# Optimization experiments

Measured on AMD Instinct MI355X. Metric: run time of the kernel, lower is better.

## Reference

```python
import jax, jax.numpy as jnp
import numpy as np

G = 8          # grid_size
DH = 32        # dim_head
EPS = 1e-5
INIT_LS = 1e-5


def setup_inputs() -> dict:
    key = jax.random.key(0)
    ks = jax.random.split(key, 8)
    B, H, W, C = 16, 128, 128, 256
    s = 1.0 / np.sqrt(C)
    return {
        "x": jax.random.normal(ks[0], (B, H, W, C), dtype=jnp.float32),
        "ln_w": jnp.ones((C,), jnp.float32),
        "ln_b": jnp.zeros((C,), jnp.float32),
        "in_proj_w": jax.random.uniform(ks[1], (3 * C, C), jnp.float32, -s, s),
        "in_proj_b": jnp.zeros((3 * C,), jnp.float32),
        "out_proj_w": jax.random.uniform(ks[2], (C, C), jnp.float32, -s, s),
        "out_proj_b": jnp.zeros((C,), jnp.float32),
        "gamma": jnp.full((C,), INIT_LS, jnp.float32),
    }


def _grid_attention(x, ln_w, ln_b, in_proj_w, in_proj_b, out_proj_w, out_proj_b, gamma):
    B, H, W, C = x.shape
    nh = C // DH
    # LayerNorm over channels
    mu = jnp.mean(x, axis=-1, keepdims=True)
    var = jnp.mean(jnp.square(x - mu), axis=-1, keepdims=True)
    x = (x - mu) * jax.lax.rsqrt(var + EPS) * ln_w + ln_b
    # grid partition: (B,G,H/G,G,W/G,C) -> (B,H/G,W/G,G,G,C) -> (N, G*G, C)
    hg, wg = H // G, W // G
    xw = x.reshape(B, G, hg, G, wg, C).transpose(0, 2, 4, 1, 3, 5)
    xw = xw.reshape(B * hg * wg, G * G, C)  # N windows of L=G*G tokens
    # MHSA (nn.MultiheadAttention semantics)
    qkv = xw @ in_proj_w.T + in_proj_b                      # (N, L, 3C)
    q, k, v = jnp.split(qkv, 3, axis=-1)
    N, L = xw.shape[0], xw.shape[1]
    q = q.reshape(N, L, nh, DH).transpose(0, 2, 1, 3)        # (N, nh, L, DH)
    k = k.reshape(N, L, nh, DH).transpose(0, 2, 1, 3)
    v = v.reshape(N, L, nh, DH).transpose(0, 2, 1, 3)
    scores = jnp.einsum("nhld,nhmd->nhlm", q, k) / np.sqrt(DH)
    attn = jax.nn.softmax(scores, axis=-1)
    out = jnp.einsum("nhlm,nhmd->nhld", attn, v)             # (N, nh, L, DH)
    out = out.transpose(0, 2, 1, 3).reshape(N, L, C)
    out = out @ out_proj_w.T + out_proj_b
    # LayerScale
    out = out * gamma
    # grid reverse: (B,H/G,W/G,G,G,C) -> (B,G,H/G,G,W/G,C) -> (B,H,W,C)
    out = out.reshape(B, hg, wg, G, G, C).transpose(0, 3, 1, 4, 2, 5)
    return out.reshape(B, H, W, C)


def reference(x, ln_w, ln_b, in_proj_w, in_proj_b, out_proj_w, out_proj_b, gamma):
    return _grid_attention(x, ln_w, ln_b, in_proj_w, in_proj_b,
                           out_proj_w, out_proj_b, gamma)
```

## Files before the change

### kernel.cpp

```cpp
#include <hip/hip_runtime.h>

typedef __attribute__((ext_vector_type(8))) short short8;
typedef __attribute__((ext_vector_type(4))) float f32x4;
typedef __attribute__((ext_vector_type(4))) unsigned short us4;

__device__ __forceinline__ unsigned short f2b(float f) {
  unsigned int u = __float_as_uint(f);
  u += 0x7FFFu + ((u >> 16) & 1u);
  return (unsigned short)(u >> 16);
}

__global__ void prep_weights(const float* __restrict__ wq,
                             const float* __restrict__ wo,
                             unsigned short* __restrict__ dst) {
  int idx = blockIdx.x * blockDim.x + threadIdx.x;
  int e = idx * 4;
  float4 v;
  if (e < 196608) v = *(const float4*)(wq + e);
  else            v = *(const float4*)(wo + (e - 196608));
  us4 o;
  o.x = f2b(v.x); o.y = f2b(v.y); o.z = f2b(v.z); o.w = f2b(v.w);
  *(us4*)(dst + e) = o;
}

__global__ __launch_bounds__(512, 4) void grid_attn(
    const float* __restrict__ x,
    const float* __restrict__ ln_w,
    const float* __restrict__ ln_b,
    const unsigned short* __restrict__ Wqkv,
    const float* __restrict__ bqkv,
    const unsigned short* __restrict__ Wout,
    const float* __restrict__ bout,
    const float* __restrict__ gamma,
    float* __restrict__ out) {

  __shared__ unsigned short ldsX[64 * 264];
  __shared__ unsigned short ldsB[8][1152];

  const int tid = threadIdx.x;
  const int w   = tid >> 6;
  const int lid = tid & 63;
  const int l16 = lid & 15;
  const int lhi = lid >> 4;

  const int n  = blockIdx.x;
  const int b  = n >> 8;
  const int wi = (n >> 4) & 15;
  const int wj = n & 15;

  {
    float4 lwv = *(const float4*)(ln_w + lid * 4);
    float4 lbv = *(const float4*)(ln_b + lid * 4);
    #pragma unroll
    for (int t = 0; t < 8; ++t) {
      int l  = w * 8 + t;
      int a  = l >> 3, cg = l & 7;
      int hh = a * 16 + wi, ww = cg * 16 + wj;
      const float4 v = *(const float4*)(x + ((size_t)((b * 128 + hh) * 128 + ww)) * 256 + lid * 4);
      float s1 = v.x + v.y + v.z + v.w;
      float s2 = v.x * v.x + v.y * v.y + v.z * v.z + v.w * v.w;
      #pragma unroll
      for (int m = 32; m >= 1; m >>= 1) {
        s1 += __shfl_xor(s1, m);
        s2 += __shfl_xor(s2, m);
      }
      float mu  = s1 * (1.0f / 256.0f);
      float var = s2 * (1.0f / 256.0f) - mu * mu;
      float rs  = rsqrtf(var + 1e-5f);
      us4 o;
      o.x = f2b((v.x - mu) * rs * lwv.x + lbv.x);
      o.y = f2b((v.y - mu) * rs * lwv.y + lbv.y);
      o.z = f2b((v.z - mu) * rs * lwv.z + lbv.z);
      o.w = f2b((v.w - mu) * rs * lwv.w + lbv.w);
      *(us4*)(&ldsX[l * 264 + lid * 4]) = o;
    }
  }
  __syncthreads();

  unsigned short* bb = &ldsB[w][0];

  f32x4 qa[2][4], ka[2][4];
  #pragma unroll
  for (int dt = 0; dt < 2; ++dt)
    #pragma unroll
    for (int tt = 0; tt < 4; ++tt) {
      qa[dt][tt] = (f32x4){0.f, 0.f, 0.f, 0.f};
      ka[dt][tt] = (f32x4){0.f, 0.f, 0.f, 0.f};
    }
  #pragma unroll
  for (int kc = 0; kc < 8; ++kc) {
    short8 xf[4];
    #pragma unroll
    for (int tt = 0; tt < 4; ++tt)
      xf[tt] = *(const short8*)(&ldsX[(tt * 16 + l16) * 264 + kc * 32 + lhi * 8]);
    short8 wq[2], wk[2];
    #pragma unroll
    for (int dt = 0; dt < 2; ++dt) {
      wq[dt] = *(const short8*)(&Wqkv[(size_t)(w * 32 + dt * 16 + l16) * 256 + kc * 32 + lhi * 8]);
      wk[dt] = *(const short8*)(&Wqkv[(size_t)(256 + w * 32 + dt * 16 + l16) * 256 + kc * 32 + lhi * 8]);
    }
    #pragma unroll
    for (int dt = 0; dt < 2; ++dt)
      #pragma unroll
      for (int tt = 0; tt < 4; ++tt) {
        qa[dt][tt] = __builtin_amdgcn_mfma_f32_16x16x32_bf16(wq[dt], xf[tt], qa[dt][tt], 0, 0, 0);
        ka[dt][tt] = __builtin_amdgcn_mfma_f32_16x16x32_bf16(wk[dt], xf[tt], ka[dt][tt], 0, 0, 0);
      }
  }

  short8 qf[4], kf[4];
  {
    f32x4 bqv[2], bkv[2];
    #pragma unroll
    for (int dt = 0; dt < 2; ++dt) {
      bqv[dt] = *(const f32x4*)(bqkv + w * 32 + dt * 16 + lhi * 4);
      bkv[dt] = *(const f32x4*)(bqkv + 256 + w * 32 + dt * 16 + lhi * 4);
    }
    #pragma unroll
    for (int tt = 0; tt < 4; ++tt) {
      #pragma unroll
      for (int dt = 0; dt < 2; ++dt)
        #pragma unroll
        for (int r = 0; r < 4; ++r)
          bb[l16 * 40 + dt * 16 + lhi * 4 + r] = f2b(qa[dt][tt][r] + bqv[dt][r]);
      qf[tt] = *(const short8*)(&bb[l16 * 40 + lhi * 8]);
    }
    #pragma unroll
    for (int tt = 0; tt < 4; ++tt) {
      #pragma unroll
      for (int dt = 0; dt < 2; ++dt)
        #pragma unroll
        for (int r = 0; r < 4; ++r)
          bb[l16 * 40 + dt * 16 + lhi * 4 + r] = f2b(ka[dt][tt][r] + bkv[dt][r]);
      kf[tt] = *(const short8*)(&bb[l16 * 40 + lhi * 8]);
    }
  }

  f32x4 sc[4][4];
  #pragma unroll
  for (int m = 0; m < 4; ++m)
    #pragma unroll
    for (int nn = 0; nn < 4; ++nn)
      sc[m][nn] = __builtin_amdgcn_mfma_f32_16x16x32_bf16(kf[m], qf[nn], (f32x4){0.f,0.f,0.f,0.f}, 0, 0, 0);

  short8 pf[4][2];
  const float scale = 0.17677669529663687f;
  #pragma unroll
  for (int nn = 0; nn < 4; ++nn) {
    float mx = sc[0][nn][0];
    #pragma unroll
    for (int m = 0; m < 4; ++m)
      #pragma unroll
      for (int r = 0; r < 4; ++r)
        mx = fmaxf(mx, sc[m][nn][r]);
    mx = fmaxf(mx, __shfl_xor(mx, 16));
    mx = fmaxf(mx, __shfl_xor(mx, 32));
    float e[4][4], sum = 0.f;
    #pragma unroll
    for (int m = 0; m < 4; ++m)
      #pragma unroll
      for (int r = 0; r < 4; ++r) {
        e[m][r] = __expf((sc[m][nn][r] - mx) * scale);
        sum += e[m][r];
      }
    sum += __shfl_xor(sum, 16);
    sum += __shfl_xor(sum, 32);
    float inv = 1.0f / sum;
    #pragma unroll
    for (int m = 0; m < 4; ++m)
      #pragma unroll
      for (int r = 0; r < 4; ++r)
        bb[l16 * 72 + m * 16 + lhi * 4 + r] = f2b(e[m][r] * inv);
    pf[nn][0] = *(const short8*)(&bb[l16 * 72 + lhi * 8]);
    pf[nn][1] = *(const short8*)(&bb[l16 * 72 + 32 + lhi * 8]);
  }

  f32x4 va[4][2];
  #pragma unroll
  for (int tt = 0; tt < 4; ++tt)
    #pragma unroll
    for (int dt = 0; dt < 2; ++dt)
      va[tt][dt] = (f32x4){0.f, 0.f, 0.f, 0.f};
  #pragma unroll
  for (int kc = 0; kc < 8; ++kc) {
    short8 xf[4];
    #pragma unroll
    for (int tt = 0; tt < 4; ++tt)
      xf[tt] = *(const short8*)(&ldsX[(tt * 16 + l16) * 264 + kc * 32 + lhi * 8]);
    short8 wv[2];
    #pragma unroll
    for (int dt = 0; dt < 2; ++dt)
      wv[dt] = *(const short8*)(&Wqkv[(size_t)(512 + w * 32 + dt * 16 + l16) * 256 + kc * 32 + lhi * 8]);
    #pragma unroll
    for (int tt = 0; tt < 4; ++tt)
      #pragma unroll
      for (int dt = 0; dt < 2; ++dt)
        va[tt][dt] = __builtin_amdgcn_mfma_f32_16x16x32_bf16(xf[tt], wv[dt], va[tt][dt], 0, 0, 0);
  }

  short8 vf[2][2];
  {
    float bvs[2];
    #pragma unroll
    for (int dt = 0; dt < 2; ++dt) bvs[dt] = bqkv[512 + w * 32 + dt * 16 + l16];
    #pragma unroll
    for (int dt = 0; dt < 2; ++dt) {
      #pragma unroll
      for (int tt = 0; tt < 4; ++tt)
        #pragma unroll
        for (int r = 0; r < 4; ++r)
          bb[l16 * 72 + tt * 16 + lhi * 4 + r] = f2b(va[tt][dt][r] + bvs[dt]);
      vf[dt][0] = *(const short8*)(&bb[l16 * 72 + lhi * 8]);
      vf[dt][1] = *(const short8*)(&bb[l16 * 72 + 32 + lhi * 8]);
    }
  }

  f32x4 oa[4][2];
  #pragma unroll
  for (int nn = 0; nn < 4; ++nn)
    #pragma unroll
    for (int dt = 0; dt < 2; ++dt)
      oa[nn][dt] = (f32x4){0.f, 0.f, 0.f, 0.f};
  #pragma unroll
  for (int kc = 0; kc < 2; ++kc)
    #pragma unroll
    for (int nn = 0; nn < 4; ++nn)
      #pragma unroll
      for (int dt = 0; dt < 2; ++dt)
        oa[nn][dt] = __builtin_amdgcn_mfma_f32_16x16x32_bf16(pf[nn][kc], vf[dt][kc], oa[nn][dt], 0, 0, 0);

  __syncthreads();

  #pragma unroll
  for (int nn = 0; nn < 4; ++nn)
    #pragma unroll
    for (int dt = 0; dt < 2; ++dt)
      #pragma unroll
      for (int r = 0; r < 4; ++r)
        ldsX[(nn * 16 + lhi * 4 + r) * 264 + w * 32 + dt * 16 + l16] = f2b(oa[nn][dt][r]);
  __syncthreads();

  f32x4 ya[4][2];
  #pragma unroll
  for (int mt = 0; mt < 4; ++mt)
    #pragma unroll
    for (int nt = 0; nt < 2; ++nt)
      ya[mt][nt] = (f32x4){0.f, 0.f, 0.f, 0.f};
  #pragma unroll
  for (int kc = 0; kc < 8; ++kc) {
    short8 af[4];
    #pragma unroll
    for (int mt = 0; mt < 4; ++mt)
      af[mt] = *(const short8*)(&ldsX[(mt * 16 + l16) * 264 + kc * 32 + lhi * 8]);
    short8 wf[2];
    #pragma unroll
    for (int nt = 0; nt < 2; ++nt)
      wf[nt] = *(const short8*)(&Wout[(size_t)(w * 32 + nt * 16 + l16) * 256 + kc * 32 + lhi * 8]);
    #pragma unroll
    for (int mt = 0; mt < 4; ++mt)
      #pragma unroll
      for (int nt = 0; nt < 2; ++nt)
        ya[mt][nt] = __builtin_amdgcn_mfma_f32_16x16x32_bf16(af[mt], wf[nt], ya[mt][nt], 0, 0, 0);
  }

  float ob0 = bout[w * 32 + l16];
  float ob1 = bout[w * 32 + 16 + l16];
  float g0  = gamma[w * 32 + l16];
  float g1  = gamma[w * 32 + 16 + l16];
  #pragma unroll
  for (int mt = 0; mt < 4; ++mt)
    #pragma unroll
    for (int r = 0; r < 4; ++r) {
      int row = mt * 16 + lhi * 4 + r;
      int a = row >> 3, cg = row & 7;
      int hh = a * 16 + wi, ww2 = cg * 16 + wj;
      float* po = out + ((size_t)((b * 128 + hh) * 128 + ww2)) * 256 + w * 32;
      po[l16]      = (ya[mt][0][r] + ob0) * g0;
      po[l16 + 16] = (ya[mt][1][r] + ob1) * g1;
    }
}

extern "C" void kernel_launch(void* const* d_in, const int* in_sizes, int n_in,
                              void* d_out, int out_size, void* d_ws, size_t ws_size,
                              hipStream_t stream) {
  const float* x    = (const float*)d_in[0];
  const float* ln_w = (const float*)d_in[1];
  const float* ln_b = (const float*)d_in[2];
  const float* ipw  = (const float*)d_in[3];
  const float* ipb  = (const float*)d_in[4];
  const float* opw  = (const float*)d_in[5];
  const float* opb  = (const float*)d_in[6];
  const float* gm   = (const float*)d_in[7];

  unsigned short* wbf = (unsigned short*)d_ws;

  prep_weights<<<256, 256, 0, stream>>>(ipw, opw, wbf);
  grid_attn<<<4096, 512, 0, stream>>>(x, ln_w, ln_b,
                                      wbf, ipb,
                                      wbf + 196608, opb,
                                      gm, (float*)d_out);
}
```

Measured before the change: 358.8 us.

## Fold LayerNorm and LayerScale into weights; replace LDS transposes with permlane swaps

LayerNorm's affine terms and gamma are now folded into the bf16 weights and precomputed bias vectors in a prep kernel. The main kernel stores raw bf16 x and applies mean/rstd as a rank-1 correction after the QKV GEMM. The per-row reductions are batched with a shuffle transpose, and the accumulator-to-operand layout changes for Q/K/P/V go through v_permlane swaps instead of per-wave LDS scratch. The attention output is computed transposed so it can be written with packed stores. Rounding x to bf16 before normalisation changes numerics and can lose accuracy when the mean is large.

```diff
diff --git a/kernel.cpp b/kernel.cpp
--- a/kernel.cpp
+++ b/kernel.cpp
@@ -1,41 +1,77 @@
 #include <hip/hip_runtime.h>
+#include <hip/hip_bf16.h>
 
 typedef __attribute__((ext_vector_type(8))) short short8;
 typedef __attribute__((ext_vector_type(4))) float f32x4;
 typedef __attribute__((ext_vector_type(4))) unsigned short us4;
+typedef __attribute__((ext_vector_type(2))) unsigned uint2v;
+
+union U8 { unsigned u[4]; short8 s; };
 
 __device__ __forceinline__ unsigned short f2b(float f) {
-  unsigned int u = __float_as_uint(f);
+  unsigned u = __float_as_uint(f);
   u += 0x7FFFu + ((u >> 16) & 1u);
   return (unsigned short)(u >> 16);
 }
-
-__global__ void prep_weights(const float* __restrict__ wq,
-                             const float* __restrict__ wo,
-                             unsigned short* __restrict__ dst) {
-  int idx = blockIdx.x * blockDim.x + threadIdx.x;
-  int e = idx * 4;
-  float4 v;
-  if (e < 196608) v = *(const float4*)(wq + e);
-  else            v = *(const float4*)(wo + (e - 196608));
-  us4 o;
-  o.x = f2b(v.x); o.y = f2b(v.y); o.z = f2b(v.z); o.w = f2b(v.w);
-  *(us4*)(dst + e) = o;
+__device__ __forceinline__ float b2f(unsigned short h) {
+  return __uint_as_float((unsigned)h << 16);
+}
+__device__ __forceinline__ unsigned pkbf(float lo, float hi) {
+  __hip_bfloat162 h = __float22bfloat162_rn(make_float2(lo, hi));
+  unsigned u; __builtin_memcpy(&u, &h, 4);
+  return u;
+}
+__device__ __forceinline__ void swp32(unsigned &a, unsigned &b) {
+  asm("v_permlane32_swap_b32 %0, %1" : "+v"(a), "+v"(b));
+}
+__device__ __forceinline__ void swp16(unsigned &a, unsigned &b) {
+  asm("v_permlane16_swap_b32 %0, %1" : "+v"(a), "+v"(b));
+}
+
+__global__ __launch_bounds__(64) void prep(
+    const float* __restrict__ wq, const float* __restrict__ wo,
+    const float* __restrict__ lnw, const float* __restrict__ lnb,
+    const float* __restrict__ bqkv, const float* __restrict__ bo,
+    const float* __restrict__ gm,
+    unsigned short* __restrict__ wbf, float* __restrict__ Sarr,
+    float* __restrict__ Carr, float* __restrict__ boG) {
+  int d = blockIdx.x, lane = threadIdx.x;
+  if (d < 768) {
+    float4 wv = *(const float4*)(wq + (size_t)d * 256 + lane * 4);
+    float4 lw = *(const float4*)(lnw + lane * 4);
+    float4 lb = *(const float4*)(lnb + lane * 4);
+    us4 o;
+    o.x = f2b(wv.x * lw.x); o.y = f2b(wv.y * lw.y);
+    o.z = f2b(wv.z * lw.z); o.w = f2b(wv.w * lw.w);
+    *(us4*)(wbf + (size_t)d * 256 + lane * 4) = o;
+    float s = b2f(o.x) + b2f(o.y) + b2f(o.z) + b2f(o.w);
+    float c = wv.x * lb.x + wv.y * lb.y + wv.z * lb.z + wv.w * lb.w;
+    #pragma unroll
+    for (int m = 32; m >= 1; m >>= 1) { s += __shfl_xor(s, m); c += __shfl_xor(c, m); }
+    if (lane == 0) { Sarr[d] = s; Carr[d] = c + bqkv[d]; }
+  } else {
+    int dd = d - 768;
+    float g = gm[dd];
+    float4 wv = *(const float4*)(wo + (size_t)dd * 256 + lane * 4);
+    us4 o;
+    o.x = f2b(wv.x * g); o.y = f2b(wv.y * g); o.z = f2b(wv.z * g); o.w = f2b(wv.w * g);
+    *(us4*)(wbf + 196608 + (size_t)dd * 256 + lane * 4) = o;
+    if (lane == 0) boG[dd] = bo[dd] * g;
+  }
 }
 
 __global__ __launch_bounds__(512, 4) void grid_attn(
     const float* __restrict__ x,
-    const float* __restrict__ ln_w,
-    const float* __restrict__ ln_b,
     const unsigned short* __restrict__ Wqkv,
-    const float* __restrict__ bqkv,
     const unsigned short* __restrict__ Wout,
-    const float* __restrict__ bout,
-    const float* __restrict__ gamma,
+    const float* __restrict__ Sarr,
+    const float* __restrict__ Carr,
+    const float* __restrict__ boG,
     float* __restrict__ out) {
 
   __shared__ unsigned short ldsX[64 * 264];
-  __shared__ unsigned short ldsB[8][1152];
+  __shared__ float ldsMu[64];
+  __shared__ float ldsRs[64];
 
   const int tid = threadIdx.x;
   const int w   = tid >> 6;
@@ -49,35 +85,54 @@
   const int wj = n & 15;
 
   {
-    float4 lwv = *(const float4*)(ln_w + lid * 4);
-    float4 lbv = *(const float4*)(ln_b + lid * 4);
+    float2 p[8];
     #pragma unroll
     for (int t = 0; t < 8; ++t) {
-      int l  = w * 8 + t;
-      int a  = l >> 3, cg = l & 7;
+      int l = w * 8 + t;
+      int a = l >> 3, cg = l & 7;
       int hh = a * 16 + wi, ww = cg * 16 + wj;
-      const float4 v = *(const float4*)(x + ((size_t)((b * 128 + hh) * 128 + ww)) * 256 + lid * 4);
-      float s1 = v.x + v.y + v.z + v.w;
-      float s2 = v.x * v.x + v.y * v.y + v.z * v.z + v.w * v.w;
-      #pragma unroll
-      for (int m = 32; m >= 1; m >>= 1) {
-        s1 += __shfl_xor(s1, m);
-        s2 += __shfl_xor(s2, m);
-      }
-      float mu  = s1 * (1.0f / 256.0f);
-      float var = s2 * (1.0f / 256.0f) - mu * mu;
-      float rs  = rsqrtf(var + 1e-5f);
-      us4 o;
-      o.x = f2b((v.x - mu) * rs * lwv.x + lbv.x);
-      o.y = f2b((v.y - mu) * rs * lwv.y + lbv.y);
-      o.z = f2b((v.z - mu) * rs * lwv.z + lbv.z);
-      o.w = f2b((v.w - mu) * rs * lwv.w + lbv.w);
-      *(us4*)(&ldsX[l * 264 + lid * 4]) = o;
+      float4 v = *(const float4*)(x + ((size_t)((b * 128 + hh) * 128 + ww)) * 256 + lid * 4);
+      p[t].x = v.x + v.y + v.z + v.w;
+      p[t].y = v.x * v.x + v.y * v.y + v.z * v.z + v.w * v.w;
+      uint2v o; o.x = pkbf(v.x, v.y); o.y = pkbf(v.z, v.w);
+      *(uint2v*)(&ldsX[l * 264 + lid * 4]) = o;
+    }
+    const int h1 = lid & 1, h2 = (lid >> 1) & 1, h4 = (lid >> 2) & 1;
+    float2 q[4];
+    #pragma unroll
+    for (int i = 0; i < 4; ++i) {
+      float sx = h1 ? p[i].x : p[i + 4].x, sy = h1 ? p[i].y : p[i + 4].y;
+      float kx = h1 ? p[i + 4].x : p[i].x, ky = h1 ? p[i + 4].y : p[i].y;
+      q[i].x = kx + __shfl_xor(sx, 1);
+      q[i].y = ky + __shfl_xor(sy, 1);
+    }
+    float2 r2[2];
+    #pragma unroll
+    for (int i = 0; i < 2; ++i) {
+      float sx = h2 ? q[i].x : q[i + 2].x, sy = h2 ? q[i].y : q[i + 2].y;
+      float kx = h2 ? q[i + 2].x : q[i].x, ky = h2 ? q[i + 2].y : q[i].y;
+      r2[i].x = kx + __shfl_xor(sx, 2);
+      r2[i].y = ky + __shfl_xor(sy, 2);
+    }
+    float fx, fy;
+    {
+      float sx = h4 ? r2[0].x : r2[1].x, sy = h4 ? r2[0].y : r2[1].y;
+      float kx = h4 ? r2[1].x : r2[0].x, ky = h4 ? r2[1].y : r2[0].y;
+      fx = kx + __shfl_xor(sx, 4);
+      fy = ky + __shfl_xor(sy, 4);
+    }
+    fx += __shfl_xor(fx, 8);  fy += __shfl_xor(fy, 8);
+    fx += __shfl_xor(fx, 16); fy += __shfl_xor(fy, 16);
+    fx += __shfl_xor(fx, 32); fy += __shfl_xor(fy, 32);
+    if (lid < 8) {
+      int T = h1 * 4 + h2 * 2 + h4;
+      float mu = fx * (1.0f / 256.0f);
+      float var = fy * (1.0f / 256.0f) - mu * mu;
+      ldsMu[w * 8 + T] = mu;
+      ldsRs[w * 8 + T] = rsqrtf(var + 1e-5f);
     }
   }
   __syncthreads();
-
-  unsigned short* bb = &ldsB[w][0];
 
   f32x4 qa[2][4], ka[2][4];
   #pragma unroll
@@ -87,52 +142,66 @@
       qa[dt][tt] = (f32x4){0.f, 0.f, 0.f, 0.f};
       ka[dt][tt] = (f32x4){0.f, 0.f, 0.f, 0.f};
     }
-  #pragma unroll
-  for (int kc = 0; kc < 8; ++kc) {
-    short8 xf[4];
-    #pragma unroll
-    for (int tt = 0; tt < 4; ++tt)
-      xf[tt] = *(const short8*)(&ldsX[(tt * 16 + l16) * 264 + kc * 32 + lhi * 8]);
-    short8 wq[2], wk[2];
-    #pragma unroll
-    for (int dt = 0; dt < 2; ++dt) {
-      wq[dt] = *(const short8*)(&Wqkv[(size_t)(w * 32 + dt * 16 + l16) * 256 + kc * 32 + lhi * 8]);
-      wk[dt] = *(const short8*)(&Wqkv[(size_t)(256 + w * 32 + dt * 16 + l16) * 256 + kc * 32 + lhi * 8]);
-    }
-    #pragma unroll
-    for (int dt = 0; dt < 2; ++dt)
+  {
+    const unsigned short* wqp = Wqkv + (size_t)(w * 32 + l16) * 256 + lhi * 8;
+    const unsigned short* wkp = wqp + 256 * 256;
+    #pragma unroll
+    for (int kc = 0; kc < 8; ++kc) {
+      short8 xf[4];
+      #pragma unroll
+      for (int tt = 0; tt < 4; ++tt)
+        xf[tt] = *(const short8*)(&ldsX[(tt * 16 + l16) * 264 + kc * 32 + lhi * 8]);
+      short8 wq0 = *(const short8*)(wqp + kc * 32);
+      short8 wq1 = *(const short8*)(wqp + 16 * 256 + kc * 32);
+      short8 wk0 = *(const short8*)(wkp + kc * 32);
+      short8 wk1 = *(const short8*)(wkp + 16 * 256 + kc * 32);
       #pragma unroll
       for (int tt = 0; tt < 4; ++tt) {
-        qa[dt][tt] = __builtin_amdgcn_mfma_f32_16x16x32_bf16(wq[dt], xf[tt], qa[dt][tt], 0, 0, 0);
-        ka[dt][tt] = __builtin_amdgcn_mfma_f32_16x16x32_bf16(wk[dt], xf[tt], ka[dt][tt], 0, 0, 0);
-      }
+        qa[0][tt] = __builtin_amdgcn_mfma_f32_16x16x32_bf16(wq0, xf[tt], qa[0][tt], 0, 0, 0);
+        qa[1][tt] = __builtin_amdgcn_mfma_f32_16x16x32_bf16(wq1, xf[tt], qa[1][tt], 0, 0, 0);
+        ka[0][tt] = __builtin_amdgcn_mfma_f32_16x16x32_bf16(wk0, xf[tt], ka[0][tt], 0, 0, 0);
+        ka[1][tt] = __builtin_amdgcn_mfma_f32_16x16x32_bf16(wk1, xf[tt], ka[1][tt], 0, 0, 0);
+      }
+    }
   }
 
   short8 qf[4], kf[4];
   {
-    f32x4 bqv[2], bkv[2];
-    #pragma unroll
-    for (int dt = 0; dt < 2; ++dt) {
-      bqv[dt] = *(const f32x4*)(bqkv + w * 32 + dt * 16 + lhi * 4);
-      bkv[dt] = *(const f32x4*)(bqkv + 256 + w * 32 + dt * 16 + lhi * 4);
-    }
+    f32x4 Sq0 = *(const f32x4*)(Sarr + w * 32 + lhi * 4);
+    f32x4 Sq1 = *(const f32x4*)(Sarr + w * 32 + 16 + lhi * 4);
+    f32x4 Cq0 = *(const f32x4*)(Carr + w * 32 + lhi * 4);
+    f32x4 Cq1 = *(const f32x4*)(Carr + w * 32 + 16 + lhi * 4);
+    f32x4 Sk0 = *(const f32x4*)(Sarr + 256 + w * 32 + lhi * 4);
+    f32x4 Sk1 = *(const f32x4*)(Sarr + 256 + w * 32 + 16 + lhi * 4);
+    f32x4 Ck0 = *(const f32x4*)(Carr + 256 + w * 32 + lhi * 4);
+    f32x4 Ck1 = *(const f32x4*)(Carr + 256 + w * 32 + 16 + lhi * 4);
     #pragma unroll
     for (int tt = 0; tt < 4; ++tt) {
-      #pragma unroll
-      for (int dt = 0; dt < 2; ++dt)
-        #pragma unroll
-        for (int r = 0; r < 4; ++r)
-          bb[l16 * 40 + dt * 16 + lhi * 4 + r] = f2b(qa[dt][tt][r] + bqv[dt][r]);
-      qf[tt] = *(const short8*)(&bb[l16 * 40 + lhi * 8]);
-    }
-    #pragma unroll
-    for (int tt = 0; tt < 4; ++tt) {
-      #pragma unroll
-      for (int dt = 0; dt < 2; ++dt)
-        #pragma unroll
-        for (int r = 0; r < 4; ++r)
-          bb[l16 * 40 + dt * 16 + lhi * 4 + r] = f2b(ka[dt][tt][r] + bkv[dt][r]);
-      kf[tt] = *(const short8*)(&bb[l16 * 40 + lhi * 8]);
+      float rs  = ldsRs[tt * 16 + l16];
+      float nmu = -ldsMu[tt * 16 + l16];
+      float e0[4], e1[4];
+      #pragma unroll
+      for (int r = 0; r < 4; ++r) {
+        e0[r] = fmaf(rs, fmaf(nmu, Sq0[r], qa[0][tt][r]), Cq0[r]);
+        e1[r] = fmaf(rs, fmaf(nmu, Sq1[r], qa[1][tt][r]), Cq1[r]);
+      }
+      unsigned a0 = pkbf(e0[0], e0[1]), a1 = pkbf(e0[2], e0[3]);
+      unsigned a2 = pkbf(e1[0], e1[1]), a3 = pkbf(e1[2], e1[3]);
+      swp32(a0, a2); swp32(a1, a3);
+      swp16(a0, a2); swp16(a1, a3);
+      U8 z; z.u[0] = a0; z.u[1] = a1; z.u[2] = a2; z.u[3] = a3;
+      qf[tt] = z.s;
+      #pragma unroll
+      for (int r = 0; r < 4; ++r) {
+        e0[r] = fmaf(rs, fmaf(nmu, Sk0[r], ka[0][tt][r]), Ck0[r]);
+        e1[r] = fmaf(rs, fmaf(nmu, Sk1[r], ka[1][tt][r]), Ck1[r]);
+      }
+      unsigned c0 = pkbf(e0[0], e0[1]), c1 = pkbf(e0[2], e0[3]);
+      unsigned c2 = pkbf(e1[0], e1[1]), c3 = pkbf(e1[2], e1[3]);
+      swp32(c0, c2); swp32(c1, c3);
+      swp16(c0, c2); swp16(c1, c3);
+      U8 y; y.u[0] = c0; y.u[1] = c1; y.u[2] = c2; y.u[3] = c3;
+      kf[tt] = y.s;
     }
   }
 
@@ -141,9 +210,9 @@
   for (int m = 0; m < 4; ++m)
     #pragma unroll
     for (int nn = 0; nn < 4; ++nn)
-      sc[m][nn] = __builtin_amdgcn_mfma_f32_16x16x32_bf16(kf[m], qf[nn], (f32x4){0.f,0.f,0.f,0.f}, 0, 0, 0);
-
-  short8 pf[4][2];
+      sc[m][nn] = __builtin_amdgcn_mfma_f32_16x16x32_bf16(kf[m], qf[nn], (f32x4){0.f, 0.f, 0.f, 0.f}, 0, 0, 0);
+
+  short8 ptf[4][2];
   const float scale = 0.17677669529663687f;
   #pragma unroll
   for (int nn = 0; nn < 4; ++nn) {
@@ -166,13 +235,19 @@
     sum += __shfl_xor(sum, 16);
     sum += __shfl_xor(sum, 32);
     float inv = 1.0f / sum;
-    #pragma unroll
-    for (int m = 0; m < 4; ++m)
-      #pragma unroll
-      for (int r = 0; r < 4; ++r)
-        bb[l16 * 72 + m * 16 + lhi * 4 + r] = f2b(e[m][r] * inv);
-    pf[nn][0] = *(const short8*)(&bb[l16 * 72 + lhi * 8]);
-    pf[nn][1] = *(const short8*)(&bb[l16 * 72 + 32 + lhi * 8]);
+    unsigned bu[8];
+    #pragma unroll
+    for (int m = 0; m < 4; ++m) {
+      bu[m * 2]     = pkbf(e[m][0] * inv, e[m][1] * inv);
+      bu[m * 2 + 1] = pkbf(e[m][2] * inv, e[m][3] * inv);
+    }
+    swp32(bu[0], bu[2]); swp32(bu[1], bu[3]); swp32(bu[4], bu[6]); swp32(bu[5], bu[7]);
+    swp16(bu[0], bu[2]); swp16(bu[1], bu[3]); swp16(bu[4], bu[6]); swp16(bu[5], bu[7]);
+    U8 z0, z1;
+    z0.u[0] = bu[0]; z0.u[1] = bu[1]; z0.u[2] = bu[2]; z0.u[3] = bu[3];
+    z1.u[0] = bu[4]; z1.u[1] = bu[5]; z1.u[2] = bu[6]; z1.u[3] = bu[7];
+    ptf[nn][0] = z0.s;
+    ptf[nn][1] = z1.s;
   }
 
   f32x4 va[4][2];
@@ -181,63 +256,84 @@
     #pragma unroll
     for (int dt = 0; dt < 2; ++dt)
       va[tt][dt] = (f32x4){0.f, 0.f, 0.f, 0.f};
-  #pragma unroll
-  for (int kc = 0; kc < 8; ++kc) {
-    short8 xf[4];
-    #pragma unroll
-    for (int tt = 0; tt < 4; ++tt)
-      xf[tt] = *(const short8*)(&ldsX[(tt * 16 + l16) * 264 + kc * 32 + lhi * 8]);
-    short8 wv[2];
-    #pragma unroll
-    for (int dt = 0; dt < 2; ++dt)
-      wv[dt] = *(const short8*)(&Wqkv[(size_t)(512 + w * 32 + dt * 16 + l16) * 256 + kc * 32 + lhi * 8]);
-    #pragma unroll
-    for (int tt = 0; tt < 4; ++tt)
-      #pragma unroll
-      for (int dt = 0; dt < 2; ++dt)
-        va[tt][dt] = __builtin_amdgcn_mfma_f32_16x16x32_bf16(xf[tt], wv[dt], va[tt][dt], 0, 0, 0);
-  }
-
-  short8 vf[2][2];
-  {
-    float bvs[2];
-    #pragma unroll
-    for (int dt = 0; dt < 2; ++dt) bvs[dt] = bqkv[512 + w * 32 + dt * 16 + l16];
+  {
+    const unsigned short* wvp = Wqkv + (size_t)(512 + w * 32 + l16) * 256 + lhi * 8;
+    #pragma unroll
+    for (int kc = 0; kc < 8; ++kc) {
+      short8 xf[4];
+      #pragma unroll
+      for (int tt = 0; tt < 4; ++tt)
+        xf[tt] = *(const short8*)(&ldsX[(tt * 16 + l16) * 264 + kc * 32 + lhi * 8]);
+      short8 wv0 = *(const short8*)(wvp + kc * 32);
+      short8 wv1 = *(const short8*)(wvp + 16 * 256 + kc * 32);
+      #pragma unroll
+      for (int tt = 0; tt < 4; ++tt) {
+        va[tt][0] = __builtin_amdgcn_mfma_f32_16x16x32_bf16(xf[tt], wv0, va[tt][0], 0, 0, 0);
+        va[tt][1] = __builtin_amdgcn_mfma_f32_16x16x32_bf16(xf[tt], wv1, va[tt][1], 0, 0, 0);
+      }
+    }
+  }
+
+  short8 vtf[2][2];
+  {
+    f32x4 rs4[4], nmu4[4];
+    #pragma unroll
+    for (int tt = 0; tt < 4; ++tt) {
+      rs4[tt] = *(const f32x4*)(&ldsRs[tt * 16 + lhi * 4]);
+      f32x4 m4 = *(const f32x4*)(&ldsMu[tt * 16 + lhi * 4]);
+      nmu4[tt] = -m4;
+    }
     #pragma unroll
     for (int dt = 0; dt < 2; ++dt) {
+      float Sv = Sarr[512 + w * 32 + dt * 16 + l16];
+      float Cv = Carr[512 + w * 32 + dt * 16 + l16];
+      float vv[4][4];
       #pragma unroll
       for (int tt = 0; tt < 4; ++tt)
         #pragma unroll
         for (int r = 0; r < 4; ++r)
-          bb[l16 * 72 + tt * 16 + lhi * 4 + r] = f2b(va[tt][dt][r] + bvs[dt]);
-      vf[dt][0] = *(const short8*)(&bb[l16 * 72 + lhi * 8]);
-      vf[dt][1] = *(const short8*)(&bb[l16 * 72 + 32 + lhi * 8]);
-    }
-  }
-
-  f32x4 oa[4][2];
+          vv[tt][r] = fmaf(rs4[tt][r], fmaf(nmu4[tt][r], Sv, va[tt][dt][r]), Cv);
+      unsigned bu[8];
+      #pragma unroll
+      for (int tt = 0; tt < 4; ++tt) {
+        bu[tt * 2]     = pkbf(vv[tt][0], vv[tt][1]);
+        bu[tt * 2 + 1] = pkbf(vv[tt][2], vv[tt][3]);
+      }
+      swp32(bu[0], bu[2]); swp32(bu[1], bu[3]); swp32(bu[4], bu[6]); swp32(bu[5], bu[7]);
+      swp16(bu[0], bu[2]); swp16(bu[1], bu[3]); swp16(bu[4], bu[6]); swp16(bu[5], bu[7]);
+      U8 z0, z1;
+      z0.u[0] = bu[0]; z0.u[1] = bu[1]; z0.u[2] = bu[2]; z0.u[3] = bu[3];
+      z1.u[0] = bu[4]; z1.u[1] = bu[5]; z1.u[2] = bu[6]; z1.u[3] = bu[7];
+      vtf[dt][0] = z0.s;
+      vtf[dt][1] = z1.s;
+    }
+  }
+
+  f32x4 ot[2][4];
+  #pragma unroll
+  for (int dt = 0; dt < 2; ++dt)
+    #pragma unroll
+    for (int nn = 0; nn < 4; ++nn)
+      ot[dt][nn] = (f32x4){0.f, 0.f, 0.f, 0.f};
+  #pragma unroll
+  for (int kc = 0; kc < 2; ++kc)
+    #pragma unroll
+    for (int dt = 0; dt < 2; ++dt)
+      #pragma unroll
+      for (int nn = 0; nn < 4; ++nn)
+        ot[dt][nn] = __builtin_amdgcn_mfma_f32_16x16x32_bf16(vtf[dt][kc], ptf[nn][kc], ot[dt][nn], 0, 0, 0);
+
+  __syncthreads();
+
   #pragma unroll
   for (int nn = 0; nn < 4; ++nn)
     #pragma unroll
-    for (int dt = 0; dt < 2; ++dt)
-      oa[nn][dt] = (f32x4){0.f, 0.f, 0.f, 0.f};
-  #pragma unroll
-  for (int kc = 0; kc < 2; ++kc)
-    #pragma unroll
-    for (int nn = 0; nn < 4; ++nn)
-      #pragma unroll
-      for (int dt = 0; dt < 2; ++dt)
-        oa[nn][dt] = __builtin_amdgcn_mfma_f32_16x16x32_bf16(pf[nn][kc], vf[dt][kc], oa[nn][dt], 0, 0, 0);
-
-  __syncthreads();
-
-  #pragma unroll
-  for (int nn = 0; nn < 4; ++nn)
-    #pragma unroll
-    for (int dt = 0; dt < 2; ++dt)
-      #pragma unroll
-      for (int r = 0; r < 4; ++r)
-        ldsX[(nn * 16 + lhi * 4 + r) * 264 + w * 32 + dt * 16 + l16] = f2b(oa[nn][dt][r]);
+    for (int dt = 0; dt < 2; ++dt) {
+      uint2v o;
+      o.x = pkbf(ot[dt][nn][0], ot[dt][nn][1]);
+      o.y = pkbf(ot[dt][nn][2], ot[dt][nn][3]);
+      *(uint2v*)(&ldsX[(nn * 16 + l16) * 264 + w * 32 + dt * 16 + lhi * 4]) = o;
+    }
   __syncthreads();
 
   f32x4 ya[4][2];
@@ -246,27 +342,26 @@
     #pragma unroll
     for (int nt = 0; nt < 2; ++nt)
       ya[mt][nt] = (f32x4){0.f, 0.f, 0.f, 0.f};
-  #pragma unroll
-  for (int kc = 0; kc < 8; ++kc) {
-    short8 af[4];
-    #pragma unroll
-    for (int mt = 0; mt < 4; ++mt)
-      af[mt] = *(const short8*)(&ldsX[(mt * 16 + l16) * 264 + kc * 32 + lhi * 8]);
-    short8 wf[2];
-    #pragma unroll
-    for (int nt = 0; nt < 2; ++nt)
-      wf[nt] = *(const short8*)(&Wout[(size_t)(w * 32 + nt * 16 + l16) * 256 + kc * 32 + lhi * 8]);
-    #pragma unroll
-    for (int mt = 0; mt < 4; ++mt)
-      #pragma unroll
-      for (int nt = 0; nt < 2; ++nt)
-        ya[mt][nt] = __builtin_amdgcn_mfma_f32_16x16x32_bf16(af[mt], wf[nt], ya[mt][nt], 0, 0, 0);
-  }
-
-  float ob0 = bout[w * 32 + l16];
-  float ob1 = bout[w * 32 + 16 + l16];
-  float g0  = gamma[w * 32 + l16];
-  float g1  = gamma[w * 32 + 16 + l16];
+  {
+    const unsigned short* wop = Wout + (size_t)(w * 32 + l16) * 256 + lhi * 8;
+    #pragma unroll
+    for (int kc = 0; kc < 8; ++kc) {
+      short8 af[4];
+      #pragma unroll
+      for (int mt = 0; mt < 4; ++mt)
+        af[mt] = *(const short8*)(&ldsX[(mt * 16 + l16) * 264 + kc * 32 + lhi * 8]);
+      short8 wf0 = *(const short8*)(wop + kc * 32);
+      short8 wf1 = *(const short8*)(wop + 16 * 256 + kc * 32);
+      #pragma unroll
+      for (int mt = 0; mt < 4; ++mt) {
+        ya[mt][0] = __builtin_amdgcn_mfma_f32_16x16x32_bf16(af[mt], wf0, ya[mt][0], 0, 0, 0);
+        ya[mt][1] = __builtin_amdgcn_mfma_f32_16x16x32_bf16(af[mt], wf1, ya[mt][1], 0, 0, 0);
+      }
+    }
+  }
+
+  float ob0 = boG[w * 32 + l16];
+  float ob1 = boG[w * 32 + 16 + l16];
   #pragma unroll
   for (int mt = 0; mt < 4; ++mt)
     #pragma unroll
@@ -275,8 +370,8 @@
       int a = row >> 3, cg = row & 7;
       int hh = a * 16 + wi, ww2 = cg * 16 + wj;
       float* po = out + ((size_t)((b * 128 + hh) * 128 + ww2)) * 256 + w * 32;
-      po[l16]      = (ya[mt][0][r] + ob0) * g0;
-      po[l16 + 16] = (ya[mt][1][r] + ob1) * g1;
+      po[l16]      = ya[mt][0][r] + ob0;
+      po[l16 + 16] = ya[mt][1][r] + ob1;
     }
 }
 
@@ -293,10 +388,12 @@
   const float* gm   = (const float*)d_in[7];
 
   unsigned short* wbf = (unsigned short*)d_ws;
-
-  prep_weights<<<256, 256, 0, stream>>>(ipw, opw, wbf);
-  grid_attn<<<4096, 512, 0, stream>>>(x, ln_w, ln_b,
-                                      wbf, ipb,
-                                      wbf + 196608, opb,
-                                      gm, (float*)d_out);
-}
+  float* Sarr = (float*)(wbf + 262144);
+  float* Carr = Sarr + 768;
+  float* boG  = Carr + 768;
+
+  prep<<<1024, 64, 0, stream>>>(ipw, opw, ln_w, ln_b, ipb, opb, gm,
+                                wbf, Sarr, Carr, boG);
+  grid_attn<<<4096, 512, 0, stream>>>(x, wbf, wbf + 196608,
+                                      Sarr, Carr, boG, (float*)d_out);
+}
```

Result: slower. 630.2 us (+75.6%).
